# Optimization experiments

Hardware: AMD Instinct MI355X
Metric: run time of the kernel (lower is better)

## Reference

```python
import jax, jax.numpy as jnp
import numpy as np

DIM = 512
HEADS = 8
HEAD_DIM = DIM // HEADS
SCALE = HEAD_DIM ** -0.5


def setup_inputs() -> dict:
    key = jax.random.key(0)
    ks = jax.random.split(key, 7)
    B, QN, N = 32, 128, 4096
    q = jax.random.normal(ks[0], (B, QN, DIM), dtype=jnp.float32)
    kv = jax.random.normal(ks[1], (B, N, DIM), dtype=jnp.float32)
    key_mask = jax.random.normal(ks[2], (B, QN, N), dtype=jnp.float32)
    Wq = jax.random.normal(ks[3], (DIM, DIM), dtype=jnp.float32) * 0.02
    Wkv = jax.random.normal(ks[4], (2 * DIM, DIM), dtype=jnp.float32) * 0.02
    Wproj = jax.random.normal(ks[5], (DIM, DIM), dtype=jnp.float32) * 0.02
    bproj = jax.random.normal(ks[6], (DIM,), dtype=jnp.float32) * 0.02
    return {"q": q, "kv": kv, "key_mask": key_mask,
            "Wq": Wq, "Wkv": Wkv, "Wproj": Wproj, "bproj": bproj}


def reference(q, kv, key_mask, Wq, Wkv, Wproj, bproj):
    B, QN, C = q.shape
    N = kv.shape[1]
    # q projection -> [B, QN, H, hd]
    qh = (q @ Wq.T).reshape(B, QN, HEADS, HEAD_DIM) * SCALE
    # kv projection -> split into k, v each [B, N, H, hd]
    kvp = kv @ Wkv.T  # [B, N, 2C]
    k = kvp[..., :C].reshape(B, N, HEADS, HEAD_DIM)
    v = kvp[..., C:].reshape(B, N, HEADS, HEAD_DIM)
    # scores [B, H, QN, N] + additive mask broadcast over heads
    attn = jnp.einsum('bqhd,bkhd->bhqk', qh, k) + key_mask[:, None]
    attn = jax.nn.softmax(attn, axis=-1)
    x = jnp.einsum('bhqk,bkhd->bqhd', attn, v).reshape(B, QN, C)
    return x @ Wproj.T + bproj
```

## Files before the change

### kernel.cpp

```cpp
#include <hip/hip_runtime.h>
#include <hip/hip_bf16.h>

typedef __attribute__((ext_vector_type(4))) float f32x4;
typedef __attribute__((ext_vector_type(8))) short bf16x8;

#define GAS __attribute__((address_space(1)))
#define LAS __attribute__((address_space(3)))

__device__ __forceinline__ unsigned int cvtpk(float lo, float hi) {
  unsigned int r;
  asm("v_cvt_pk_bf16_f32 %0, %1, %2" : "=v"(r) : "v"(lo), "v"(hi));
  return r;
}
__device__ __forceinline__ unsigned short f2bf(float f) { return (unsigned short)cvtpk(f, f); }
__device__ __forceinline__ f32x4 mfma16(bf16x8 a, bf16x8 b, f32x4 c) {
  return __builtin_amdgcn_mfma_f32_16x16x32_bf16(a, b, c, 0, 0, 0);
}
__device__ __forceinline__ void gl_lds16(const unsigned short* g, unsigned short* l) {
  __builtin_amdgcn_global_load_lds((const GAS unsigned short*)g, (LAS unsigned short*)l, 16, 0, 0);
}
__device__ __forceinline__ void memfence_sched() { asm volatile("" ::: "memory"); }

__global__ __launch_bounds__(256)
void cvt_f32_bf16(const float* __restrict__ in, unsigned short* __restrict__ out, int n8) {
  for (int i = blockIdx.x * blockDim.x + threadIdx.x; i < n8; i += gridDim.x * blockDim.x) {
    const float4 a = *reinterpret_cast<const float4*>(in + (size_t)i * 8);
    const float4 b = *reinterpret_cast<const float4*>(in + (size_t)i * 8 + 4);
    uint4 o;
    o.x = cvtpk(a.x, a.y); o.y = cvtpk(a.z, a.w);
    o.z = cvtpk(b.x, b.y); o.w = cvtpk(b.z, b.w);
    *reinterpret_cast<uint4*>(out + (size_t)i * 8) = o;
  }
}

template<int MODE>
__global__ __launch_bounds__(512, 1)
void gemm8p(const unsigned short* __restrict__ Ag, const unsigned short* __restrict__ Bg,
            void* __restrict__ Cg, const float* __restrict__ bias, int ntn, size_t ldc)
{
  __shared__ unsigned short sm[65536];
  const int t = threadIdx.x, lane = t & 63, w = t >> 6;
  const int lo = lane & 15, hi = lane >> 4;
  const int wm = w >> 2, wn = w & 3;
  const int nwg = gridDim.x, bid = blockIdx.x;
  const int id = (bid & 7) * (nwg >> 3) + (bid >> 3);
  const int row0 = (id / ntn) * 256, col0 = (id % ntn) * 256;

  const int srow = t >> 2;
  const int scol = ((t & 3) ^ ((t >> 3) & 3)) * 8;
  const unsigned short* aS = Ag + (size_t)(row0 + srow) * 512 + scol;
  const unsigned short* bS = Bg + (size_t)(col0 + srow) * 512 + scol;
  const int wbase = w * 512;

  auto STAGE_A = [&](int kt) {
    const int bf = kt & 3;
    gl_lds16(aS + kt * 32,         &sm[bf * 8192 + wbase]);
    gl_lds16(aS + kt * 32 + 65536, &sm[bf * 8192 + 4096 + wbase]);
  };
  auto STAGE_B = [&](int kt) {
    const int bf = kt & 3;
    gl_lds16(bS + kt * 32,         &sm[32768 + bf * 8192 + wbase]);
    gl_lds16(bS + kt * 32 + 65536, &sm[32768 + bf * 8192 + 4096 + wbase]);
  };

  f32x4 acc[8][4] = {};
  const int fc = (hi ^ ((lo >> 1) & 3)) * 8;

  STAGE_A(0); STAGE_B(0); STAGE_A(1); STAGE_B(1); STAGE_A(2); STAGE_B(2);
  memfence_sched();
  asm volatile("s_waitcnt vmcnt(8)" ::: "memory");
  __builtin_amdgcn_s_barrier();
  memfence_sched();

  #pragma unroll
  for (int kt = 0; kt < 16; ++kt) {
    const unsigned short* aB = &sm[(kt & 3) * 8192];
    const unsigned short* bB = &sm[32768 + (kt & 3) * 8192];

    bf16x8 bfr[4], af[4];
    #pragma unroll
    for (int nj = 0; nj < 4; ++nj)
      bfr[nj] = *reinterpret_cast<const bf16x8*>(&bB[(wn * 64 + nj * 16 + lo) * 32 + fc]);
    #pragma unroll
    for (int mi = 0; mi < 4; ++mi)
      af[mi] = *reinterpret_cast<const bf16x8*>(&aB[(wm * 128 + mi * 16 + lo) * 32 + fc]);
    if (kt <= 12) STAGE_A(kt + 3);
    memfence_sched();
    __builtin_amdgcn_s_barrier();
    memfence_sched();
    __builtin_amdgcn_s_setprio(1);
    #pragma unroll
    for (int mi = 0; mi < 4; ++mi)
      #pragma unroll
      for (int nj = 0; nj < 4; ++nj)
        acc[mi][nj] = mfma16(af[mi], bfr[nj], acc[mi][nj]);
    __builtin_amdgcn_s_setprio(0);
    __builtin_amdgcn_s_barrier();
    memfence_sched();

    #pragma unroll
    for (int mi = 0; mi < 4; ++mi)
      af[mi] = *reinterpret_cast<const bf16x8*>(&aB[((wm * 128) + (mi + 4) * 16 + lo) * 32 + fc]);
    if (kt <= 12) STAGE_B(kt + 3);
    memfence_sched();
    __builtin_amdgcn_s_barrier();
    memfence_sched();
    __builtin_amdgcn_s_setprio(1);
    #pragma unroll
    for (int mi = 0; mi < 4; ++mi)
      #pragma unroll
      for (int nj = 0; nj < 4; ++nj)
        acc[mi + 4][nj] = mfma16(af[mi], bfr[nj], acc[mi + 4][nj]);
    __builtin_amdgcn_s_setprio(0);
    if (kt <= 12)      { asm volatile("s_waitcnt vmcnt(8)" ::: "memory"); }
    else if (kt == 13) { asm volatile("s_waitcnt vmcnt(4)" ::: "memory"); }
    else if (kt == 14) { asm volatile("s_waitcnt vmcnt(0)" ::: "memory"); }
    if (kt < 15) { __builtin_amdgcn_s_barrier(); memfence_sched(); }
  }

  if constexpr (MODE == 1) {
    __syncthreads();
    unsigned short* Wb = &sm[w * 8192];
    #pragma unroll
    for (int mi = 0; mi < 8; ++mi)
      #pragma unroll
      for (int nj = 0; nj < 4; ++nj)
        #pragma unroll
        for (int r = 0; r < 4; ++r) {
          const int row = mi * 16 + hi * 4 + r;
          const int cst = ((nj * 2 + (lo >> 3)) ^ (row & 7)) * 8 + (lo & 7);
          Wb[row * 64 + cst] = f2bf(acc[mi][nj][r]);
        }
    asm volatile("s_waitcnt lgkmcnt(0)" ::: "memory");
    memfence_sched();
    #pragma unroll
    for (int it = 0; it < 16; ++it) {
      const int row = it * 8 + (lane >> 3);
      const int sc = ((lane & 7) ^ (row & 7)) * 8;
      const bf16x8 vrow = *reinterpret_cast<const bf16x8*>(&Wb[row * 64 + sc]);
      const size_t gm = (size_t)row0 + wm * 128 + row;
      *reinterpret_cast<bf16x8*>((unsigned short*)Cg + gm * ldc + col0 + wn * 64 +
                                 (lane & 7) * 8) = vrow;
    }
  } else {
    #pragma unroll
    for (int mi = 0; mi < 8; ++mi) {
      #pragma unroll
      for (int r = 0; r < 4; ++r) {
        const size_t gm = (size_t)row0 + wm * 128 + mi * 16 + hi * 4 + r;
        #pragma unroll
        for (int nj = 0; nj < 4; ++nj) {
          const int gn = col0 + wn * 64 + nj * 16 + lo;
          const float v = acc[mi][nj][r];
          if constexpr (MODE == 0)
            ((unsigned short*)Cg)[gm * ldc + gn] = f2bf(v * 0.125f);
          else
            ((float*)Cg)[gm * ldc + gn] = v + bias[gn];
        }
      }
    }
  }
}

__global__ __launch_bounds__(256)
void attn_fwd(const unsigned short* __restrict__ qh,
              const unsigned short* __restrict__ kbuf,
              const unsigned short* __restrict__ vT,
              const float* __restrict__ mask,
              float* __restrict__ opart, float* __restrict__ ml)
{
  __shared__ unsigned short Ks[64 * 64];
  __shared__ unsigned short Vs[64 * 64];
  __shared__ unsigned short Ps[4][16 * 64];
  const int bid = blockIdx.x;
  const int xcd = bid & 7, g = bid >> 3;
  const int b = (g >> 6) * 8 + xcd;
  const int sub = g & 63;
  const int h = sub >> 3, qhalf = (sub >> 2) & 1, c = sub & 3;
  const int n0 = c * 1024;
  const int bh2 = (b * 8 + h) * 2 + qhalf;
  const int t = threadIdx.x, lane = t & 63, w = t >> 6;
  const int hi = lane >> 4, lo = lane & 15;
  const int q0 = qhalf * 64 + w * 16;

  bf16x8 aq[2];
  #pragma unroll
  for (int kk = 0; kk < 2; ++kk)
    aq[kk] = *reinterpret_cast<const bf16x8*>(
        qh + (size_t)(b * 128 + q0 + lo) * 512 + h * 64 + kk * 32 + hi * 8);

  float mrow[4], lrow[4];
  #pragma unroll
  for (int i = 0; i < 4; ++i) { mrow[i] = -1e30f; lrow[i] = 0.f; }
  f32x4 o[4] = {};

  const unsigned short* kp = kbuf + ((size_t)b * 4096 + n0) * 512 + h * 64;
  const unsigned short* vp = vT + (size_t)(h * 64) * 131072 + (size_t)b * 4096 + n0;
  const float* mp = mask + ((size_t)(b * 128 + q0)) * 4096 + n0;

  for (int nt = 0; nt < 16; ++nt) {
    {
      const int r = t >> 3, cc = t & 7;
      *reinterpret_cast<uint4*>(&Ks[r * 64 + ((cc ^ (r & 7)) << 3)]) =
          *reinterpret_cast<const uint4*>(kp + (size_t)(nt * 64 + r) * 512 + (cc << 3));
      *reinterpret_cast<uint4*>(&Ks[(r + 32) * 64 + ((cc ^ (r & 7)) << 3)]) =
          *reinterpret_cast<const uint4*>(kp + (size_t)(nt * 64 + r + 32) * 512 + (cc << 3));
      *reinterpret_cast<uint4*>(&Vs[r * 64 + ((cc ^ (r & 7)) << 3)]) =
          *reinterpret_cast<const uint4*>(vp + (size_t)r * 131072 + nt * 64 + (cc << 3));
      *reinterpret_cast<uint4*>(&Vs[(r + 32) * 64 + ((cc ^ (r & 7)) << 3)]) =
          *reinterpret_cast<const uint4*>(vp + (size_t)(r + 32) * 131072 + nt * 64 + (cc << 3));
    }
    __syncthreads();

    f32x4 s[4] = {};
    __builtin_amdgcn_s_setprio(1);
    #pragma unroll
    for (int ni = 0; ni < 4; ++ni) {
      #pragma unroll
      for (int kk = 0; kk < 2; ++kk) {
        const bf16x8 kf = *reinterpret_cast<const bf16x8*>(
            &Ks[(ni * 16 + lo) * 64 + ((kk * 32 + hi * 8) ^ ((lo & 7) << 3))]);
        s[ni] = mfma16(aq[kk], kf, s[ni]);
      }
    }
    __builtin_amdgcn_s_setprio(0);
    #pragma unroll
    for (int ni = 0; ni < 4; ++ni)
      #pragma unroll
      for (int r = 0; r < 4; ++r)
        s[ni][r] += mp[(size_t)(hi * 4 + r) * 4096 + nt * 64 + ni * 16 + lo];

    #pragma unroll
    for (int r = 0; r < 4; ++r) {
      float mx = fmaxf(fmaxf(s[0][r], s[1][r]), fmaxf(s[2][r], s[3][r]));
      #pragma unroll
      for (int off = 1; off < 16; off <<= 1)
        mx = fmaxf(mx, __shfl_xor(mx, off, 64));
      const float mnew = fmaxf(mrow[r], mx);
      const float corr = __expf(mrow[r] - mnew);
      mrow[r] = mnew;
      float ls = 0.f;
      #pragma unroll
      for (int ni = 0; ni < 4; ++ni) {
        const float p = __expf(s[ni][r] - mnew);
        s[ni][r] = p; ls += p;
      }
      #pragma unroll
      for (int off = 1; off < 16; off <<= 1)
        ls += __shfl_xor(ls, off, 64);
      lrow[r] = lrow[r] * corr + ls;
      #pragma unroll
      for (int di = 0; di < 4; ++di)
        o[di][r] *= corr;
    }

    #pragma unroll
    for (int ni = 0; ni < 4; ++ni)
      #pragma unroll
      for (int r = 0; r < 4; ++r) {
        const int rp = hi * 4 + r;
        Ps[w][rp * 64 + ((ni * 16 + lo) ^ ((rp & 7) << 3))] = f2bf(s[ni][r]);
      }

    __builtin_amdgcn_s_setprio(1);
    #pragma unroll
    for (int kk = 0; kk < 2; ++kk) {
      const bf16x8 pa = *reinterpret_cast<const bf16x8*>(
          &Ps[w][lo * 64 + ((kk * 32 + hi * 8) ^ ((lo & 7) << 3))]);
      #pragma unroll
      for (int di = 0; di < 4; ++di) {
        const bf16x8 vf = *reinterpret_cast<const bf16x8*>(
            &Vs[(di * 16 + lo) * 64 + ((kk * 32 + hi * 8) ^ ((lo & 7) << 3))]);
        o[di] = mfma16(pa, vf, o[di]);
      }
    }
    __builtin_amdgcn_s_setprio(0);
    __syncthreads();
  }

  const size_t pbase = ((size_t)bh2 * 4 + c) * 64;
  #pragma unroll
  for (int di = 0; di < 4; ++di)
    #pragma unroll
    for (int r = 0; r < 4; ++r)
      opart[(pbase + (w * 16 + hi * 4 + r)) * 64 + di * 16 + lo] = o[di][r];
  if (lo == 0) {
    #pragma unroll
    for (int r = 0; r < 4; ++r) {
      const int qq = w * 16 + hi * 4 + r;
      ml[(((size_t)bh2 * 4 + c) * 2 + 0) * 64 + qq] = mrow[r];
      ml[(((size_t)bh2 * 4 + c) * 2 + 1) * 64 + qq] = lrow[r];
    }
  }
}

__global__ __launch_bounds__(256)
void attn_combine(const float* __restrict__ opart, const float* __restrict__ ml,
                  unsigned short* __restrict__ xb)
{
  const int bh2 = blockIdx.x;
  const int b = bh2 >> 4, h = (bh2 >> 1) & 7, qhalf = bh2 & 1;
  const int t = threadIdx.x;
  const int q = t >> 2, dg = t & 3;

  float m[4], l[4];
  #pragma unroll
  for (int c = 0; c < 4; ++c) {
    m[c] = ml[(((size_t)bh2 * 4 + c) * 2 + 0) * 64 + q];
    l[c] = ml[(((size_t)bh2 * 4 + c) * 2 + 1) * 64 + q];
  }
  const float M = fmaxf(fmaxf(m[0], m[1]), fmaxf(m[2], m[3]));
  float sc[4], L = 0.f;
  #pragma unroll
  for (int c = 0; c < 4; ++c) { sc[c] = __expf(m[c] - M); L += sc[c] * l[c]; }
  const float inv = 1.f / L;

  float4 acc[4] = {};
  #pragma unroll
  for (int c = 0; c < 4; ++c) {
    const float* base = opart + (((size_t)bh2 * 4 + c) * 64 + q) * 64 + dg * 16;
    #pragma unroll
    for (int j = 0; j < 4; ++j) {
      const float4 v = *reinterpret_cast<const float4*>(base + j * 4);
      acc[j].x = fmaf(sc[c], v.x, acc[j].x);
      acc[j].y = fmaf(sc[c], v.y, acc[j].y);
      acc[j].z = fmaf(sc[c], v.z, acc[j].z);
      acc[j].w = fmaf(sc[c], v.w, acc[j].w);
    }
  }
  unsigned short* dst = xb + ((size_t)b * 128 + qhalf * 64 + q) * 512 + h * 64 + dg * 16;
  uint4 o1, o2;
  o1.x = cvtpk(acc[0].x * inv, acc[0].y * inv); o1.y = cvtpk(acc[0].z * inv, acc[0].w * inv);
  o1.z = cvtpk(acc[1].x * inv, acc[1].y * inv); o1.w = cvtpk(acc[1].z * inv, acc[1].w * inv);
  o2.x = cvtpk(acc[2].x * inv, acc[2].y * inv); o2.y = cvtpk(acc[2].z * inv, acc[2].w * inv);
  o2.z = cvtpk(acc[3].x * inv, acc[3].y * inv); o2.w = cvtpk(acc[3].z * inv, acc[3].w * inv);
  *reinterpret_cast<uint4*>(dst) = o1;
  *reinterpret_cast<uint4*>(dst + 8) = o2;
}

extern "C" void kernel_launch(void* const* d_in, const int* in_sizes, int n_in,
                              void* d_out, int out_size, void* d_ws, size_t ws_size,
                              hipStream_t stream) {
  const float* q     = (const float*)d_in[0];
  const float* kv    = (const float*)d_in[1];
  const float* mask  = (const float*)d_in[2];
  const float* Wq    = (const float*)d_in[3];
  const float* Wkv   = (const float*)d_in[4];
  const float* Wproj = (const float*)d_in[5];
  const float* bproj = (const float*)d_in[6];
  float* out = (float*)d_out;

  char* ws = (char*)d_ws;
  unsigned short* kbuf   = (unsigned short*)ws;
  unsigned short* vTb    = (unsigned short*)(ws + 134217728ULL);
  unsigned short* kvbfc  = (unsigned short*)(ws + 268435456ULL);
  unsigned short* qbf    = kvbfc;
  float*          opart  = (float*)(ws + 268435456ULL);
  float*          mlb    = (float*)(ws + 301989888ULL);
  unsigned short* xb     = (unsigned short*)(ws + 303038464ULL);
  unsigned short* qhb    = (unsigned short*)(ws + 335544320ULL);
  unsigned short* Wqb    = (unsigned short*)(ws + 339738624ULL);
  unsigned short* Wkvb   = (unsigned short*)(ws + 340262912ULL);
  unsigned short* Wprojb = (unsigned short*)(ws + 341311488ULL);

  cvt_f32_bf16<<<128, 256, 0, stream>>>(Wq, Wqb, 512 * 512 / 8);
  cvt_f32_bf16<<<256, 256, 0, stream>>>(Wkv, Wkvb, 1024 * 512 / 8);
  cvt_f32_bf16<<<128, 256, 0, stream>>>(Wproj, Wprojb, 512 * 512 / 8);

  cvt_f32_bf16<<<256, 256, 0, stream>>>(q, qbf, 4096 * 512 / 8);
  gemm8p<0><<<32, 512, 0, stream>>>(qbf, Wqb, qhb, nullptr, 2, 512);

  for (int c = 0; c < 2; ++c) {
    cvt_f32_bf16<<<2048, 256, 0, stream>>>(kv + (size_t)c * 65536 * 512, kvbfc,
                                           65536 * 512 / 8);
    gemm8p<1><<<512, 512, 0, stream>>>(kvbfc, Wkvb,
                                       kbuf + (size_t)c * 65536 * 512, nullptr, 2, 512);
    gemm8p<1><<<512, 512, 0, stream>>>(Wkvb + 512 * 512, kvbfc,
                                       vTb + (size_t)c * 65536, nullptr, 256, 131072);
  }

  attn_fwd<<<2048, 256, 0, stream>>>(qhb, kbuf, vTb, mask, opart, mlb);
  attn_combine<<<512, 256, 0, stream>>>(opart, mlb, xb);
  gemm8p<2><<<32, 512, 0, stream>>>(xb, Wprojb, out, bproj, 2, 512);
}
```

Baseline: 448.1 us.

## Restructure GEMM main loop to K-tile 64 with double buffering

The 256x256 bf16 GEMM now stages 64-wide K tiles into a two-slot LDS ring instead of 32-wide tiles into a four-slot ring, and uses an 8-way XOR swizzle to match. Each iteration runs two K sub-steps, each issuing a full 8x4 MFMA block per wave, and prefetches both A and B tiles for two steps ahead. This halves the number of loop iterations and barrier rounds per output tile. In exchange, prefetch depth drops from three stages to two, and the code adds an explicit lgkmcnt wait before each MFMA batch.

Measured after the change: 437.4 us. 2.4% less time.

```diff
diff --git a/kernel.cpp b/kernel.cpp
--- a/kernel.cpp
+++ b/kernel.cpp
@@ -35,7 +35,7 @@
 
 template<int MODE>
 __global__ __launch_bounds__(512, 1)
-void gemm8p(const unsigned short* __restrict__ Ag, const unsigned short* __restrict__ Bg,
+void gemm8k(const unsigned short* __restrict__ Ag, const unsigned short* __restrict__ Bg,
             void* __restrict__ Cg, const float* __restrict__ bias, int ntn, size_t ldc)
 {
   __shared__ unsigned short sm[65536];
@@ -46,76 +46,69 @@
   const int id = (bid & 7) * (nwg >> 3) + (bid >> 3);
   const int row0 = (id / ntn) * 256, col0 = (id % ntn) * 256;
 
-  const int srow = t >> 2;
-  const int scol = ((t & 3) ^ ((t >> 3) & 3)) * 8;
+  const int srow = t >> 3;
+  const int scol = ((t & 7) ^ (srow & 7)) * 8;
   const unsigned short* aS = Ag + (size_t)(row0 + srow) * 512 + scol;
   const unsigned short* bS = Bg + (size_t)(col0 + srow) * 512 + scol;
-  const int wbase = w * 512;
+  const int tofs = t * 8;
 
   auto STAGE_A = [&](int kt) {
-    const int bf = kt & 3;
-    gl_lds16(aS + kt * 32,         &sm[bf * 8192 + wbase]);
-    gl_lds16(aS + kt * 32 + 65536, &sm[bf * 8192 + 4096 + wbase]);
+    unsigned short* dst = &sm[(kt & 1) * 16384];
+    #pragma unroll
+    for (int i = 0; i < 4; ++i)
+      gl_lds16(aS + (size_t)i * 64 * 512 + kt * 64, dst + i * 4096 + tofs - (lane * 8));
   };
   auto STAGE_B = [&](int kt) {
-    const int bf = kt & 3;
-    gl_lds16(bS + kt * 32,         &sm[32768 + bf * 8192 + wbase]);
-    gl_lds16(bS + kt * 32 + 65536, &sm[32768 + bf * 8192 + 4096 + wbase]);
+    unsigned short* dst = &sm[32768 + (kt & 1) * 16384];
+    #pragma unroll
+    for (int i = 0; i < 4; ++i)
+      gl_lds16(bS + (size_t)i * 64 * 512 + kt * 64, dst + i * 4096 + tofs - (lane * 8));
   };
 
   f32x4 acc[8][4] = {};
-  const int fc = (hi ^ ((lo >> 1) & 3)) * 8;
-
-  STAGE_A(0); STAGE_B(0); STAGE_A(1); STAGE_B(1); STAGE_A(2); STAGE_B(2);
+
+  STAGE_A(0); STAGE_B(0); STAGE_A(1); STAGE_B(1);
   memfence_sched();
   asm volatile("s_waitcnt vmcnt(8)" ::: "memory");
   __builtin_amdgcn_s_barrier();
   memfence_sched();
 
   #pragma unroll
-  for (int kt = 0; kt < 16; ++kt) {
-    const unsigned short* aB = &sm[(kt & 3) * 8192];
-    const unsigned short* bB = &sm[32768 + (kt & 3) * 8192];
-
-    bf16x8 bfr[4], af[4];
-    #pragma unroll
-    for (int nj = 0; nj < 4; ++nj)
-      bfr[nj] = *reinterpret_cast<const bf16x8*>(&bB[(wn * 64 + nj * 16 + lo) * 32 + fc]);
-    #pragma unroll
-    for (int mi = 0; mi < 4; ++mi)
-      af[mi] = *reinterpret_cast<const bf16x8*>(&aB[(wm * 128 + mi * 16 + lo) * 32 + fc]);
-    if (kt <= 12) STAGE_A(kt + 3);
+  for (int kt = 0; kt < 8; ++kt) {
+    const unsigned short* aB = &sm[(kt & 1) * 16384 + wm * 8192];
+    const unsigned short* bB = &sm[32768 + (kt & 1) * 16384 + (wn >> 1) * 8192];
+    const int brow = (wn & 1) * 64;
+
+    #pragma unroll
+    for (int ks = 0; ks < 2; ++ks) {
+      const int fcol = ((ks * 4 + hi) ^ (lo & 7)) * 8;
+      bf16x8 bfr[4], afr[8];
+      #pragma unroll
+      for (int nj = 0; nj < 4; ++nj)
+        bfr[nj] = *reinterpret_cast<const bf16x8*>(&bB[(brow + nj * 16 + lo) * 64 + fcol]);
+      #pragma unroll
+      for (int mi = 0; mi < 8; ++mi)
+        afr[mi] = *reinterpret_cast<const bf16x8*>(&aB[(mi * 16 + lo) * 64 + fcol]);
+      memfence_sched();
+      __builtin_amdgcn_s_barrier();
+      memfence_sched();
+      asm volatile("s_waitcnt lgkmcnt(0)" ::: "memory");
+      __builtin_amdgcn_s_setprio(1);
+      #pragma unroll
+      for (int mi = 0; mi < 8; ++mi)
+        #pragma unroll
+        for (int nj = 0; nj < 4; ++nj)
+          acc[mi][nj] = mfma16(afr[mi], bfr[nj], acc[mi][nj]);
+      __builtin_amdgcn_s_setprio(0);
+      __builtin_amdgcn_s_barrier();
+      memfence_sched();
+    }
+
+    if (kt <= 5) { STAGE_A(kt + 2); STAGE_B(kt + 2); }
     memfence_sched();
-    __builtin_amdgcn_s_barrier();
-    memfence_sched();
-    __builtin_amdgcn_s_setprio(1);
-    #pragma unroll
-    for (int mi = 0; mi < 4; ++mi)
-      #pragma unroll
-      for (int nj = 0; nj < 4; ++nj)
-        acc[mi][nj] = mfma16(af[mi], bfr[nj], acc[mi][nj]);
-    __builtin_amdgcn_s_setprio(0);
-    __builtin_amdgcn_s_barrier();
-    memfence_sched();
-
-    #pragma unroll
-    for (int mi = 0; mi < 4; ++mi)
-      af[mi] = *reinterpret_cast<const bf16x8*>(&aB[((wm * 128) + (mi + 4) * 16 + lo) * 32 + fc]);
-    if (kt <= 12) STAGE_B(kt + 3);
-    memfence_sched();
-    __builtin_amdgcn_s_barrier();
-    memfence_sched();
-    __builtin_amdgcn_s_setprio(1);
-    #pragma unroll
-    for (int mi = 0; mi < 4; ++mi)
-      #pragma unroll
-      for (int nj = 0; nj < 4; ++nj)
-        acc[mi + 4][nj] = mfma16(af[mi], bfr[nj], acc[mi + 4][nj]);
-    __builtin_amdgcn_s_setprio(0);
-    if (kt <= 12)      { asm volatile("s_waitcnt vmcnt(8)" ::: "memory"); }
-    else if (kt == 13) { asm volatile("s_waitcnt vmcnt(4)" ::: "memory"); }
-    else if (kt == 14) { asm volatile("s_waitcnt vmcnt(0)" ::: "memory"); }
-    if (kt < 15) { __builtin_amdgcn_s_barrier(); memfence_sched(); }
+    if (kt <= 5)      { asm volatile("s_waitcnt vmcnt(8)" ::: "memory"); }
+    else if (kt == 6) { asm volatile("s_waitcnt vmcnt(0)" ::: "memory"); }
+    if (kt < 7) { __builtin_amdgcn_s_barrier(); memfence_sched(); }
   }
 
   if constexpr (MODE == 1) {
@@ -368,18 +361,18 @@
   cvt_f32_bf16<<<128, 256, 0, stream>>>(Wproj, Wprojb, 512 * 512 / 8);
 
   cvt_f32_bf16<<<256, 256, 0, stream>>>(q, qbf, 4096 * 512 / 8);
-  gemm8p<0><<<32, 512, 0, stream>>>(qbf, Wqb, qhb, nullptr, 2, 512);
+  gemm8k<0><<<32, 512, 0, stream>>>(qbf, Wqb, qhb, nullptr, 2, 512);
 
   for (int c = 0; c < 2; ++c) {
     cvt_f32_bf16<<<2048, 256, 0, stream>>>(kv + (size_t)c * 65536 * 512, kvbfc,
                                            65536 * 512 / 8);
-    gemm8p<1><<<512, 512, 0, stream>>>(kvbfc, Wkvb,
+    gemm8k<1><<<512, 512, 0, stream>>>(kvbfc, Wkvb,
                                        kbuf + (size_t)c * 65536 * 512, nullptr, 2, 512);
-    gemm8p<1><<<512, 512, 0, stream>>>(Wkvb + 512 * 512, kvbfc,
+    gemm8k<1><<<512, 512, 0, stream>>>(Wkvb + 512 * 512, kvbfc,
                                        vTb + (size_t)c * 65536, nullptr, 256, 131072);
   }
 
   attn_fwd<<<2048, 256, 0, stream>>>(qhb, kbuf, vTb, mask, opart, mlb);
   attn_combine<<<512, 256, 0, stream>>>(opart, mlb, xb);
-  gemm8p<2><<<32, 512, 0, stream>>>(xb, Wprojb, out, bproj, 2, 512);
-}
+  gemm8k<2><<<32, 512, 0, stream>>>(xb, Wprojb, out, bproj, 2, 512);
+}
```
